# Kernel optimization log

Measured on AMD Instinct MI355X. Metric: run time of the kernel, lower is better.

The kernel has to match this reference:

```python
import jax, jax.numpy as jnp
import numpy as np

HID = 2048 * 3  # infl_ratio = 3
EPS = 1e-5
P_DROP = 0.5


def sign_ste(x):
    # straight-through binarization: sign in fwd, identity in bwd
    return x + jax.lax.stop_gradient(jnp.sign(x) - x)


def batchnorm(x, g, b):
    # training-mode BatchNorm1d: batch stats, biased variance
    m = jnp.mean(x, axis=0)
    v = jnp.mean((x - m) ** 2, axis=0)
    return g * (x - m) / jnp.sqrt(v + EPS) + b


def hardtanh(x):
    return jnp.clip(x, -1.0, 1.0)


def dropout(x, u):
    # u ~ U[0,1); keep where u >= p, scale by 1/(1-p)
    return jnp.where(u >= P_DROP, x / (1.0 - P_DROP), 0.0)


def setup_inputs() -> dict:
    key = jax.random.key(0)
    ks = jax.random.split(key, 16)
    B = 512
    d = {}
    d['x'] = jax.random.normal(ks[0], (B, 784), dtype=jnp.float32)
    d['drop_mask_bin'] = jax.random.uniform(ks[1], (B, HID), dtype=jnp.float32)
    d['drop_mask_real'] = jax.random.uniform(ks[2], (B, HID), dtype=jnp.float32)
    s1 = 1.0 / np.sqrt(784)
    sh = 1.0 / np.sqrt(HID)
    d['w1'] = jax.random.uniform(ks[3], (HID, 784), jnp.float32, -s1, s1)
    d['b1'] = jax.random.uniform(ks[4], (HID,), jnp.float32, -s1, s1)
    d['w2'] = jax.random.uniform(ks[5], (HID, HID), jnp.float32, -sh, sh)
    d['b2'] = jax.random.uniform(ks[6], (HID,), jnp.float32, -sh, sh)
    d['w3'] = jax.random.uniform(ks[7], (HID, HID), jnp.float32, -sh, sh)
    d['b3'] = jax.random.uniform(ks[8], (HID,), jnp.float32, -sh, sh)
    d['w4'] = jax.random.uniform(ks[9], (10, HID), jnp.float32, -sh, sh)
    d['b4'] = jax.random.uniform(ks[10], (10,), jnp.float32, -sh, sh)
    for i, k in zip((1, 2, 3), (ks[11], ks[12], ks[13])):
        d[f'g{i}'] = jnp.ones((HID,), jnp.float32)
        d[f'be{i}'] = jnp.zeros((HID,), jnp.float32)
    return d


def reference(x, drop_mask_bin, drop_mask_real, w1, b1, w2, b2, w3, b3, w4, b4,
              g1, be1, g2, be2, g3, be3):
    sg = jax.lax.stop_gradient
    # layer 1: input dim 784 -> input NOT binarized; weights binarized
    Bout1 = x @ sign_ste(w1).T + b1
    Rout1 = sg(x @ w1.T + b1)
    Bout1 = hardtanh(batchnorm(Bout1, g1, be1))
    Rout1 = sg(hardtanh(batchnorm(Rout1, g1, be1)))
    # layer 2: binarize activations and weights on binary path
    Bout2 = sign_ste(Bout1) @ sign_ste(w2).T + b2
    Rout2 = sg(Rout1 @ w2.T + b2)
    Bout2 = hardtanh(batchnorm(Bout2, g2, be2))
    Rout2 = sg(hardtanh(batchnorm(Rout2, g2, be2)))
    # layer 3 + dropout
    Bout3 = sign_ste(Bout2) @ sign_ste(w3).T + b3
    Rout3 = sg(Rout2 @ w3.T + b3)
    Bout3 = hardtanh(batchnorm(dropout(Bout3, drop_mask_bin), g3, be3))
    Rout3 = sg(hardtanh(batchnorm(dropout(Rout3, drop_mask_real), g3, be3)))
    # classifier (real-valued Linear)
    out = Bout3 @ w4.T + b4
    logp = jax.nn.log_softmax(out, axis=1)
    return (logp, out, Bout1, Rout1, Bout2, Rout2, Bout3, Rout3)
```

## Files before the change

### kernel.cpp

```cpp
#include <hip/hip_runtime.h>


typedef _Float16 f16x8 __attribute__((ext_vector_type(8)));
typedef _Float16 f16x4 __attribute__((ext_vector_type(4)));
typedef float f32x4 __attribute__((ext_vector_type(4)));
typedef int i32x4 __attribute__((ext_vector_type(4)));

#define MFMA16(a, b, c) __builtin_amdgcn_mfma_f32_16x16x32_f16((a), (b), (c), 0, 0, 0)
#define MFMAI8K32(a, b, c) __builtin_amdgcn_mfma_i32_16x16x32_i8((a), (b), (c), 0, 0, 0)
#define MFMAI8K64(a, b, c) __builtin_amdgcn_mfma_i32_16x16x64_i8((a), (b), (c), 0, 0, 0)

#define HIDC 6144
#define BATCH 512

#define OFF_XH    0ull
#define OFF_Z1LO  851968ull
#define OFF_SB8   13434880ull
#define OFF_RF    16580608ull
#define OFF_STATS 22872064ull
#define OFF_PPART 23068672ull
#define OFF_ZPB   24641536ull
#define OFF_ZPR   37224448ull
#define OFF_W1V   49807360ull
#define OFF_WV    60030976ull
#define OFF_WS8   135528448ull
#define WS_NEED   173277184ull

#define A8_STRIDE 425984ull

__device__ __forceinline__ void load_lds16(const void* g, char* lds) {
  __builtin_amdgcn_global_load_lds((const __attribute__((address_space(1))) void*)g,
                                   (__attribute__((address_space(3))) void*)lds, 16, 0, 0);
}

__global__ __launch_bounds__(256) void k_prep_x(const float* __restrict__ x,
                                                _Float16* __restrict__ xh) {
  int idx = blockIdx.x * 256 + threadIdx.x;
  if (idx >= 512 * 208) return;
  int row = idx / 208, c4 = idx - row * 208;
  f16x4 h;
  if (c4 < 196) {
    float4 v = *(const float4*)(x + (size_t)row * 784 + c4 * 4);
    h[0] = (_Float16)v.x; h[1] = (_Float16)v.y; h[2] = (_Float16)v.z; h[3] = (_Float16)v.w;
  } else {
    h[0] = (_Float16)0.f; h[1] = (_Float16)0.f; h[2] = (_Float16)0.f; h[3] = (_Float16)0.f;
  }
  *(f16x4*)(xh + (size_t)row * 832 + c4 * 4) = h;
}

__global__ __launch_bounds__(256) void k_quant_x(const float* __restrict__ x,
                                                 char* __restrict__ a8) {
  int idx = blockIdx.x * 256 + threadIdx.x;
  if (idx >= 512 * 832) return;
  int row = idx / 832, k = idx - row * 832;
  float v = (k < 784) ? x[(size_t)row * 784 + k] : 0.f;
  int q = (int)lrintf(v * 16777216.0f);
  int d0 = ((q + 128) & 255) - 128; q = (q - d0) >> 8;
  int d1 = ((q + 128) & 255) - 128; q = (q - d1) >> 8;
  int d2 = ((q + 128) & 255) - 128; q = (q - d2) >> 8;
  a8[idx] = (char)d0;
  a8[A8_STRIDE + idx] = (char)d1;
  a8[2 * A8_STRIDE + idx] = (char)d2;
  a8[3 * A8_STRIDE + idx] = (char)q;
}

__global__ __launch_bounds__(256) void k_sign_w1(const float* __restrict__ w,
                                                 char* __restrict__ s1) {
  int idx = blockIdx.x * 256 + threadIdx.x;
  if (idx >= 6144 * 832) return;
  int r = idx / 832, k = idx - r * 832;
  char s = 0;
  if (k < 784) {
    float v = w[(size_t)r * 784 + k];
    s = v > 0.f ? 1 : (v < 0.f ? -1 : 0);
  }
  s1[idx] = s;
}

__global__ __launch_bounds__(256) void k_conv_w1(const float* __restrict__ w,
                                                 _Float16* __restrict__ wv) {
  int idx = blockIdx.x * 256 + threadIdx.x;
  if (idx >= 6144 * 104) return;
  int r = idx / 104, c8 = idx - r * 104;
  f16x8 hv;
  if (c8 < 98) {
    const float* s = w + (size_t)r * 784 + c8 * 8;
    float4 v0 = *(const float4*)s;
    float4 v1 = *(const float4*)(s + 4);
    float a[8] = {v0.x, v0.y, v0.z, v0.w, v1.x, v1.y, v1.z, v1.w};
#pragma unroll
    for (int e = 0; e < 8; ++e) hv[e] = (_Float16)a[e];
  } else {
#pragma unroll
    for (int e = 0; e < 8; ++e) hv[e] = (_Float16)0.f;
  }
  *(f16x8*)(wv + (size_t)r * 832 + c8 * 8) = hv;
}

__global__ __launch_bounds__(256) void k_conv_w23(const float* __restrict__ w,
                                                  _Float16* __restrict__ wv,
                                                  char* __restrict__ ws8) {
  int idx = blockIdx.x * 256 + threadIdx.x;
  size_t o8 = (size_t)idx * 8;
  const float* s = w + o8;
  float4 v0 = *(const float4*)s;
  float4 v1 = *(const float4*)(s + 4);
  float a[8] = {v0.x, v0.y, v0.z, v0.w, v1.x, v1.y, v1.z, v1.w};
  f16x8 hv;
  unsigned long long sbits = 0;
#pragma unroll
  for (int e = 0; e < 8; ++e) {
    hv[e] = (_Float16)a[e];
    char sg = a[e] > 0.f ? 1 : (a[e] < 0.f ? -1 : 0);
    sbits |= ((unsigned long long)(unsigned char)sg) << (8 * e);
  }
  *(f16x8*)(wv + o8) = hv;
  *(unsigned long long*)(ws8 + o8) = sbits;
}

__global__ __launch_bounds__(256) void k_gemm_i8(const char* __restrict__ a8,
                                                 const char* __restrict__ s1,
                                                 int* __restrict__ D0,
                                                 int* __restrict__ D1,
                                                 int* __restrict__ D2,
                                                 int* __restrict__ D3) {
  __shared__ __align__(16) char smem[16384];
  const int z = blockIdx.z;
  const char* A = a8 + (size_t)z * A8_STRIDE;
  int* C = D0;
  if (z == 1) C = D1;
  if (z == 2) C = D2;
  if (z == 3) C = D3;
  const int t = threadIdx.x;
  const int lane = t & 63, wid = t >> 6;
  const int wm = wid >> 1, wn = wid & 1;
  const int bn = blockIdx.x, bm = blockIdx.y;

  i32x4 acc[4][4];
#pragma unroll
  for (int mf = 0; mf < 4; ++mf)
#pragma unroll
    for (int nf = 0; nf < 4; ++nf) acc[mf][nf] = (i32x4){0, 0, 0, 0};

  for (int kt = 0; kt < 13; ++kt) {
    const int k0 = kt * 64;
#pragma unroll
    for (int i = 0; i < 2; ++i) {
      int p = i * 256 + t;
      int r = p >> 2, c16 = p & 3;
      load_lds16(A + (size_t)(bm * 128 + r) * 832 + k0 + c16 * 16, smem + p * 16);
    }
#pragma unroll
    for (int i = 0; i < 2; ++i) {
      int p = i * 256 + t;
      int r = p >> 2, c16 = p & 3;
      load_lds16(s1 + (size_t)(bn * 128 + r) * 832 + k0 + c16 * 16, smem + 8192 + p * 16);
    }
    __syncthreads();
#pragma unroll
    for (int kk = 0; kk < 2; ++kk) {
      long av[4], bv[4];
#pragma unroll
      for (int mf = 0; mf < 4; ++mf) {
        int r = wm * 64 + mf * 16 + (lane & 15);
        av[mf] = *(const long*)(smem + r * 64 + kk * 32 + (lane >> 4) * 8);
      }
#pragma unroll
      for (int nf = 0; nf < 4; ++nf) {
        int r = wn * 64 + nf * 16 + (lane & 15);
        bv[nf] = *(const long*)(smem + 8192 + r * 64 + kk * 32 + (lane >> 4) * 8);
      }
#pragma unroll
      for (int mf = 0; mf < 4; ++mf)
#pragma unroll
        for (int nf = 0; nf < 4; ++nf) acc[mf][nf] = MFMAI8K32(av[mf], bv[nf], acc[mf][nf]);
    }
    __syncthreads();
  }
#pragma unroll
  for (int mf = 0; mf < 4; ++mf)
#pragma unroll
    for (int nf = 0; nf < 4; ++nf) {
      int col = bn * 128 + wn * 64 + nf * 16 + (lane & 15);
      int row0 = bm * 128 + wm * 64 + mf * 16 + ((lane >> 4) << 2);
#pragma unroll
      for (int rr = 0; rr < 4; ++rr) {
        C[(size_t)(row0 + rr) * HIDC + col] = acc[mf][nf][rr];
      }
    }
}

__global__ __launch_bounds__(256) void k_combine1(const int* __restrict__ D0,
                                                  const int* __restrict__ D1,
                                                  const int* __restrict__ D2,
                                                  const int* __restrict__ D3,
                                                  float* __restrict__ Zhi,
                                                  float* __restrict__ Zlo) {
  size_t i4 = ((size_t)blockIdx.x * 256 + threadIdx.x) * 4;
  i32x4 v0 = *(const i32x4*)(D0 + i4);
  i32x4 v1 = *(const i32x4*)(D1 + i4);
  i32x4 v2 = *(const i32x4*)(D2 + i4);
  i32x4 v3 = *(const i32x4*)(D3 + i4);
  float4 hi, lo;
  float* hp = &hi.x;
  float* lp = &lo.x;
#pragma unroll
  for (int e = 0; e < 4; ++e) {
    double zv = (((double)v3[e] * 256.0 + (double)v2[e]) * 256.0 + (double)v1[e]) * 256.0 +
                (double)v0[e];
    zv *= (1.0 / 16777216.0);
    float h = (float)zv;
    hp[e] = h;
    lp[e] = (float)(zv - (double)h);
  }
  *(float4*)(Zhi + i4) = hi;
  *(float4*)(Zlo + i4) = lo;
}

struct MixJob {
  const void* A;
  const void* B;
  float* C;
  int K;
  int kstart;
  int ksteps;
  int is8;
};
struct Mix4 { MixJob j[4]; };

__global__ __launch_bounds__(256) void k_gemm_mix(Mix4 P) {
  __shared__ __align__(16) char smem[32768];
  MixJob J = P.j[0];
  if (blockIdx.z == 1) J = P.j[1];
  if (blockIdx.z == 2) J = P.j[2];
  if (blockIdx.z == 3) J = P.j[3];
  const int t = threadIdx.x;
  const int lane = t & 63, wid = t >> 6;
  const int wm = wid >> 1, wn = wid & 1;
  const int bn = blockIdx.x, bm = blockIdx.y;
  const size_t K = (size_t)J.K;

  if (J.is8) {
    const char* A = (const char*)J.A;
    const char* B = (const char*)J.B;
    i32x4 acc[4][4];
#pragma unroll
    for (int mf = 0; mf < 4; ++mf)
#pragma unroll
      for (int nf = 0; nf < 4; ++nf) acc[mf][nf] = (i32x4){0, 0, 0, 0};

    for (int kt = 0; kt < J.ksteps; ++kt) {
      const int k0 = J.kstart + kt * 128;
#pragma unroll
      for (int i = 0; i < 4; ++i) {
        int p = i * 256 + t;
        int r = p >> 3, c16 = p & 7;
        load_lds16(A + (size_t)(bm * 128 + r) * K + k0 + c16 * 16, smem + p * 16);
      }
#pragma unroll
      for (int i = 0; i < 4; ++i) {
        int p = i * 256 + t;
        int r = p >> 3, c16 = p & 7;
        load_lds16(B + (size_t)(bn * 128 + r) * K + k0 + c16 * 16, smem + 16384 + p * 16);
      }
      __syncthreads();
#pragma unroll
      for (int kk = 0; kk < 2; ++kk) {
        i32x4 av[4], bv[4];
#pragma unroll
        for (int mf = 0; mf < 4; ++mf) {
          int r = wm * 64 + mf * 16 + (lane & 15);
          av[mf] = *(const i32x4*)(smem + r * 128 + kk * 64 + (lane >> 4) * 16);
        }
#pragma unroll
        for (int nf = 0; nf < 4; ++nf) {
          int r = wn * 64 + nf * 16 + (lane & 15);
          bv[nf] = *(const i32x4*)(smem + 16384 + r * 128 + kk * 64 + (lane >> 4) * 16);
        }
#pragma unroll
        for (int mf = 0; mf < 4; ++mf)
#pragma unroll
          for (int nf = 0; nf < 4; ++nf) acc[mf][nf] = MFMAI8K64(av[mf], bv[nf], acc[mf][nf]);
      }
      __syncthreads();
    }
#pragma unroll
    for (int mf = 0; mf < 4; ++mf)
#pragma unroll
      for (int nf = 0; nf < 4; ++nf) {
        int col = bn * 128 + wn * 64 + nf * 16 + (lane & 15);
        int row0 = bm * 128 + wm * 64 + mf * 16 + ((lane >> 4) << 2);
#pragma unroll
        for (int rr = 0; rr < 4; ++rr) {
          J.C[(size_t)(row0 + rr) * HIDC + col] = (float)acc[mf][nf][rr];
        }
      }
  } else {
    const _Float16* A = (const _Float16*)J.A;
    const _Float16* B = (const _Float16*)J.B;
    f32x4 acc[4][4];
#pragma unroll
    for (int mf = 0; mf < 4; ++mf)
#pragma unroll
      for (int nf = 0; nf < 4; ++nf) acc[mf][nf] = (f32x4){0.f, 0.f, 0.f, 0.f};

    for (int kt = 0; kt < J.ksteps; ++kt) {
      const int k0 = J.kstart + kt * 64;
#pragma unroll
      for (int i = 0; i < 4; ++i) {
        int p = i * 256 + t;
        int r = p >> 3, c16 = p & 7;
        load_lds16(A + (size_t)(bm * 128 + r) * K + k0 + c16 * 8, smem + p * 16);
      }
#pragma unroll
      for (int i = 0; i < 4; ++i) {
        int p = i * 256 + t;
        int r = p >> 3, c16 = p & 7;
        load_lds16(B + (size_t)(bn * 128 + r) * K + k0 + c16 * 8, smem + 16384 + p * 16);
      }
      __syncthreads();
#pragma unroll
      for (int kk = 0; kk < 2; ++kk) {
        f16x8 av[4], bv[4];
#pragma unroll
        for (int mf = 0; mf < 4; ++mf) {
          int r = wm * 64 + mf * 16 + (lane & 15);
          av[mf] = *(const f16x8*)(smem + r * 128 + kk * 64 + (lane >> 4) * 16);
        }
#pragma unroll
        for (int nf = 0; nf < 4; ++nf) {
          int r = wn * 64 + nf * 16 + (lane & 15);
          bv[nf] = *(const f16x8*)(smem + 16384 + r * 128 + kk * 64 + (lane >> 4) * 16);
        }
#pragma unroll
        for (int mf = 0; mf < 4; ++mf)
#pragma unroll
          for (int nf = 0; nf < 4; ++nf) acc[mf][nf] = MFMA16(av[mf], bv[nf], acc[mf][nf]);
      }
      __syncthreads();
    }
#pragma unroll
    for (int mf = 0; mf < 4; ++mf)
#pragma unroll
      for (int nf = 0; nf < 4; ++nf) {
        int col = bn * 128 + wn * 64 + nf * 16 + (lane & 15);
        int row0 = bm * 128 + wm * 64 + mf * 16 + ((lane >> 4) << 2);
#pragma unroll
        for (int rr = 0; rr < 4; ++rr) {
          J.C[(size_t)(row0 + rr) * HIDC + col] = acc[mf][nf][rr];
        }
      }
  }
}

struct StJob { const float* Z; const float* Zpart; const float* msk; };
struct St2 { StJob j[2]; const float* bias; int dodrop; double* ppart; };

__global__ __launch_bounds__(256) void k_stats_part(St2 P) {
  __shared__ double sm[4][64];
  __shared__ double sq[4][64];
  const int z = blockIdx.z;
  StJob J = z ? P.j[1] : P.j[0];
  const int li = threadIdx.x & 63, rg = threadIdx.x >> 6;
  const int col = blockIdx.x * 64 + li;
  const double bb = P.dodrop ? (double)P.bias[col] : 0.0;
  double s = 0.0, s2 = 0.0;
#pragma unroll 4
  for (int rr = 0; rr < 16; ++rr) {
    int r = blockIdx.y * 64 + rg * 16 + rr;
    size_t i = (size_t)r * HIDC + col;
    double v = (double)J.Z[i];
    if (J.Zpart) v += (double)J.Zpart[i];
    if (P.dodrop) v = (J.msk[i] >= 0.5f) ? 2.0 * (v + bb) : 0.0;
    s += v;
    s2 += v * v;
  }
  sm[rg][li] = s;
  sq[rg][li] = s2;
  __syncthreads();
  if (rg == 0) {
    double S = sm[0][li] + sm[1][li] + sm[2][li] + sm[3][li];
    double S2 = sq[0][li] + sq[1][li] + sq[2][li] + sq[3][li];
    size_t o = ((size_t)(z * 8 + blockIdx.y) * 2) * HIDC + col;
    P.ppart[o] = S;
    P.ppart[o + HIDC] = S2;
  }
}

__global__ __launch_bounds__(256) void k_stats_fin(const double* __restrict__ ppart,
                                                   double* __restrict__ stats) {
  const int z = blockIdx.z;
  const int c = blockIdx.x * 256 + threadIdx.x;
  double S = 0.0, S2 = 0.0;
#pragma unroll
  for (int y = 0; y < 8; ++y) {
    size_t o = ((size_t)(z * 8 + y) * 2) * HIDC + c;
    S += ppart[o];
    S2 += ppart[o + HIDC];
  }
  double m = S / 512.0;
  double var = S2 / 512.0 - m * m;
  stats[z * 2 * HIDC + c] = m;
  stats[z * 2 * HIDC + HIDC + c] = 1.0 / sqrt(var + 1e-5);
}

struct BnJob { float* Z; const float* Zpart; void* aux; const float* msk; int auxmode; };
struct Bn2 {
  BnJob j[2];
  const double* stats;
  const float* g; const float* be; const float* bias;
  int dodrop;
};

__global__ __launch_bounds__(256) void k_bn2(Bn2 P) {
  const int z = blockIdx.z;
  BnJob J = z ? P.j[1] : P.j[0];
  const double* m_arr = P.stats + (size_t)z * 2 * HIDC;
  const double* r_arr = m_arr + HIDC;
  int idx = blockIdx.x * 256 + threadIdx.x;
  int row = idx / 1536;
  int c4 = (idx - row * 1536) * 4;
  size_t base = (size_t)row * HIDC + c4;
  float4 zv = *(const float4*)(J.Z + base);
  float zz[4] = {zv.x, zv.y, zv.z, zv.w};
  float zl[4] = {0.f, 0.f, 0.f, 0.f};
  if (J.Zpart) {
    float4 t4 = *(const float4*)(J.Zpart + base);
    zl[0] = t4.x; zl[1] = t4.y; zl[2] = t4.z; zl[3] = t4.w;
  }
  float mk[4] = {1.f, 1.f, 1.f, 1.f};
  if (P.dodrop) {
    float4 t4 = *(const float4*)(J.msk + base);
    mk[0] = t4.x; mk[1] = t4.y; mk[2] = t4.z; mk[3] = t4.w;
  }
  float o[4];
  f16x4 a4;
  int sbits = 0;
#pragma unroll
  for (int e = 0; e < 4; ++e) {
    int c = c4 + e;
    double v = (double)zz[e] + (double)zl[e];
    if (P.dodrop) v = (mk[e] >= 0.5f) ? 2.0 * (v + (double)P.bias[c]) : 0.0;
    double bnv = (double)P.g[c] * ((v - m_arr[c]) * r_arr[c]) + (double)P.be[c];
    bnv = bnv > 1.0 ? 1.0 : (bnv < -1.0 ? -1.0 : bnv);
    o[e] = (float)bnv;
    char sg = bnv > 0.0 ? 1 : (bnv < 0.0 ? -1 : 0);
    sbits |= ((int)(unsigned char)sg) << (8 * e);
    a4[e] = (_Float16)o[e];
  }
  float4 ov = {o[0], o[1], o[2], o[3]};
  *(float4*)(J.Z + base) = ov;
  if (J.auxmode == 0) *(int*)((char*)J.aux + base) = sbits;
  if (J.auxmode == 1) *(f16x4*)((_Float16*)J.aux + base) = a4;
}

__global__ __launch_bounds__(256) void k_head(const float* __restrict__ B3,
                                              const float* __restrict__ w4,
                                              const float* __restrict__ b4,
                                              float* __restrict__ out,
                                              float* __restrict__ logp) {
  const int row = blockIdx.x, t = threadIdx.x;
  float acc[10];
#pragma unroll
  for (int j = 0; j < 10; ++j) acc[j] = 0.f;
  const float* a = B3 + (size_t)row * HIDC;
  for (int k4 = t; k4 < 1536; k4 += 256) {
    float4 av = *(const float4*)(a + k4 * 4);
#pragma unroll
    for (int j = 0; j < 10; ++j) {
      float4 wv = *(const float4*)(w4 + (size_t)j * HIDC + k4 * 4);
      acc[j] += av.x * wv.x + av.y * wv.y + av.z * wv.z + av.w * wv.w;
    }
  }
#pragma unroll
  for (int j = 0; j < 10; ++j)
    for (int off = 32; off; off >>= 1) acc[j] += __shfl_down(acc[j], off);
  __shared__ float sred[4][10];
  int wid = t >> 6, ln = t & 63;
  if (ln == 0)
#pragma unroll
    for (int j = 0; j < 10; ++j) sred[wid][j] = acc[j];
  __syncthreads();
  if (t == 0) {
    double o[10];
    double mx = -1e300;
#pragma unroll
    for (int j = 0; j < 10; ++j) {
      o[j] = (double)sred[0][j] + sred[1][j] + sred[2][j] + sred[3][j] + (double)b4[j];
      mx = o[j] > mx ? o[j] : mx;
    }
    double s = 0.0;
#pragma unroll
    for (int j = 0; j < 10; ++j) s += exp(o[j] - mx);
    double l = log(s) + mx;
#pragma unroll
    for (int j = 0; j < 10; ++j) {
      out[row * 10 + j] = (float)o[j];
      logp[row * 10 + j] = (float)(o[j] - l);
    }
  }
}

extern "C" void kernel_launch(void* const* d_in, const int* in_sizes, int n_in,
                              void* d_out, int out_size, void* d_ws, size_t ws_size,
                              hipStream_t stream) {
  const float* x   = (const float*)d_in[0];
  const float* mkb = (const float*)d_in[1];
  const float* mkr = (const float*)d_in[2];
  const float* w1  = (const float*)d_in[3];
  const float* w2  = (const float*)d_in[5];
  const float* w3  = (const float*)d_in[7];
  const float* b3  = (const float*)d_in[8];
  const float* w4  = (const float*)d_in[9];
  const float* b4  = (const float*)d_in[10];
  const float* g1  = (const float*)d_in[11]; const float* be1 = (const float*)d_in[12];
  const float* g2  = (const float*)d_in[13]; const float* be2 = (const float*)d_in[14];
  const float* g3  = (const float*)d_in[15]; const float* be3 = (const float*)d_in[16];

  float* outp = (float*)d_out;
  float* logp = outp;
  float* outo = outp + 5120;
  float* B1 = outp + 10240;
  float* R1 = outp + 3155968;
  float* B2 = outp + 6301696;
  float* R2 = outp + 9447424;
  float* B3 = outp + 12593152;
  float* R3 = outp + 15738880;

  char* ws = (char*)d_ws;
  _Float16* xh  = (_Float16*)(ws + OFF_XH);
  float* z1lo   = (float*)(ws + OFF_Z1LO);
  char* sB8     = (char*)(ws + OFF_SB8);
  _Float16* rF  = (_Float16*)(ws + OFF_RF);
  double* stats = (double*)(ws + OFF_STATS);
  double* ppart = (double*)(ws + OFF_PPART);
  float* zpb    = (float*)(ws + OFF_ZPB);
  float* zpr    = (float*)(ws + OFF_ZPR);
  _Float16* w1v = (_Float16*)(ws + OFF_W1V);
  _Float16* wv  = (_Float16*)(ws + OFF_WV);
  char* ws8     = (char*)(ws + OFF_WS8);
  char* a8 = (char*)(ws + OFF_WS8);
  char* s1 = (char*)(ws + OFF_WS8 + 2097152ull);
  int* D0 = (int*)(ws + OFF_ZPB);
  int* D1 = (int*)(ws + OFF_ZPR);
  int* D2 = (int*)(ws + OFF_WV);
  int* D3 = (int*)(ws + OFF_WV + 12582912ull);

  k_prep_x<<<416, 256, 0, stream>>>(x, xh);
  k_conv_w1<<<2496, 256, 0, stream>>>(w1, w1v);
  k_quant_x<<<1664, 256, 0, stream>>>(x, a8);
  k_sign_w1<<<19968, 256, 0, stream>>>(w1, s1);
  k_gemm_i8<<<dim3(48, 4, 4), 256, 0, stream>>>(a8, s1, D0, D1, D2, D3);
  k_combine1<<<3072, 256, 0, stream>>>(D0, D1, D2, D3, B1, z1lo);
  {
    Mix4 P{};
    P.j[0] = {xh, w1v, R1, 832, 0, 13, 0};
    P.j[1] = P.j[0]; P.j[2] = P.j[0]; P.j[3] = P.j[0];
    k_gemm_mix<<<dim3(48, 4, 1), 256, 0, stream>>>(P);
  }
  {
    St2 S{}; S.j[0] = {B1, z1lo, nullptr}; S.j[1] = {R1, nullptr, nullptr};
    S.bias = nullptr; S.dodrop = 0; S.ppart = ppart;
    k_stats_part<<<dim3(96, 8, 2), 256, 0, stream>>>(S);
    k_stats_fin<<<dim3(24, 1, 2), 256, 0, stream>>>(ppart, stats);
    Bn2 B{}; B.j[0] = {B1, z1lo, sB8, nullptr, 0}; B.j[1] = {R1, nullptr, rF, nullptr, 1};
    B.stats = stats; B.g = g1; B.be = be1; B.bias = nullptr; B.dodrop = 0;
    k_bn2<<<dim3(3072, 1, 2), 256, 0, stream>>>(B);
  }
  k_conv_w23<<<18432, 256, 0, stream>>>(w2, wv, ws8);
  {
    Mix4 P{};
    P.j[0] = {sB8, ws8, B2, HIDC, 0, 24, 1};
    P.j[1] = {sB8, ws8, zpb, HIDC, 3072, 24, 1};
    P.j[2] = {rF, wv, R2, HIDC, 0, 48, 0};
    P.j[3] = {rF, wv, zpr, HIDC, 3072, 48, 0};
    k_gemm_mix<<<dim3(48, 4, 4), 256, 0, stream>>>(P);
  }
  {
    St2 S{}; S.j[0] = {B2, zpb, nullptr}; S.j[1] = {R2, zpr, nullptr};
    S.bias = nullptr; S.dodrop = 0; S.ppart = ppart;
    k_stats_part<<<dim3(96, 8, 2), 256, 0, stream>>>(S);
    k_stats_fin<<<dim3(24, 1, 2), 256, 0, stream>>>(ppart, stats);
    Bn2 B{}; B.j[0] = {B2, zpb, sB8, nullptr, 0}; B.j[1] = {R2, zpr, rF, nullptr, 1};
    B.stats = stats; B.g = g2; B.be = be2; B.bias = nullptr; B.dodrop = 0;
    k_bn2<<<dim3(3072, 1, 2), 256, 0, stream>>>(B);
  }
  k_conv_w23<<<18432, 256, 0, stream>>>(w3, wv, ws8);
  {
    Mix4 P{};
    P.j[0] = {sB8, ws8, B3, HIDC, 0, 24, 1};
    P.j[1] = {sB8, ws8, zpb, HIDC, 3072, 24, 1};
    P.j[2] = {rF, wv, R3, HIDC, 0, 48, 0};
    P.j[3] = {rF, wv, zpr, HIDC, 3072, 48, 0};
    k_gemm_mix<<<dim3(48, 4, 4), 256, 0, stream>>>(P);
  }
  {
    St2 S{}; S.j[0] = {B3, zpb, mkb}; S.j[1] = {R3, zpr, mkr};
    S.bias = b3; S.dodrop = 1; S.ppart = ppart;
    k_stats_part<<<dim3(96, 8, 2), 256, 0, stream>>>(S);
    k_stats_fin<<<dim3(24, 1, 2), 256, 0, stream>>>(ppart, stats);
    Bn2 B{}; B.j[0] = {B3, zpb, nullptr, mkb, 2}; B.j[1] = {R3, zpr, nullptr, mkr, 2};
    B.stats = stats; B.g = g3; B.be = be3; B.bias = b3; B.dodrop = 1;
    k_bn2<<<dim3(3072, 1, 2), 256, 0, stream>>>(B);
  }
  k_head<<<512, 256, 0, stream>>>(B3, w4, b4, outo, logp);
}
```

Measured before the change: 564.1 us.

## Merge layer-1 GEMMs into mixed launch and split real-path K four ways

Layer-1 input prep is fused so one kernel quantizes x and converts it to fp16, and one kernel writes both the sign and the fp16 copy of w1. The separate int8 GEMM kernel is dropped; its four limb GEMMs now run as jobs of the generic mixed GEMM kernel, with K padded to 896, in the same launch as the fp16 real-path GEMM. For layers 2 and 3 the real-path GEMM is split into four K-chunks instead of two, which doubles the number of blocks in flight. The cost is two more fp32 partial buffers that the stats and batchnorm kernels must read and sum, plus a larger workspace.

```diff
diff --git a/kernel.cpp b/kernel.cpp
--- a/kernel.cpp
+++ b/kernel.cpp
@@ -7,7 +7,6 @@
 typedef int i32x4 __attribute__((ext_vector_type(4)));
 
 #define MFMA16(a, b, c) __builtin_amdgcn_mfma_f32_16x16x32_f16((a), (b), (c), 0, 0, 0)
-#define MFMAI8K32(a, b, c) __builtin_amdgcn_mfma_i32_16x16x32_i8((a), (b), (c), 0, 0, 0)
 #define MFMAI8K64(a, b, c) __builtin_amdgcn_mfma_i32_16x16x64_i8((a), (b), (c), 0, 0, 0)
 
 #define HIDC 6144
@@ -21,38 +20,26 @@
 #define OFF_PPART 23068672ull
 #define OFF_ZPB   24641536ull
 #define OFF_ZPR   37224448ull
-#define OFF_W1V   49807360ull
-#define OFF_WV    60030976ull
-#define OFF_WS8   135528448ull
-#define WS_NEED   173277184ull
-
-#define A8_STRIDE 425984ull
+#define OFF_ZPR2  49807360ull
+#define OFF_ZPR3  62390272ull
+#define OFF_W1V   74973184ull
+#define OFF_WV    85196800ull
+#define OFF_WS8   160694272ull
+#define WS_NEED   198443008ull
+
+#define A8_STRIDE 458752ull
 
 __device__ __forceinline__ void load_lds16(const void* g, char* lds) {
   __builtin_amdgcn_global_load_lds((const __attribute__((address_space(1))) void*)g,
                                    (__attribute__((address_space(3))) void*)lds, 16, 0, 0);
 }
 
-__global__ __launch_bounds__(256) void k_prep_x(const float* __restrict__ x,
-                                                _Float16* __restrict__ xh) {
+__global__ __launch_bounds__(256) void k_prep_xq(const float* __restrict__ x,
+                                                 char* __restrict__ a8,
+                                                 _Float16* __restrict__ xh) {
   int idx = blockIdx.x * 256 + threadIdx.x;
-  if (idx >= 512 * 208) return;
-  int row = idx / 208, c4 = idx - row * 208;
-  f16x4 h;
-  if (c4 < 196) {
-    float4 v = *(const float4*)(x + (size_t)row * 784 + c4 * 4);
-    h[0] = (_Float16)v.x; h[1] = (_Float16)v.y; h[2] = (_Float16)v.z; h[3] = (_Float16)v.w;
-  } else {
-    h[0] = (_Float16)0.f; h[1] = (_Float16)0.f; h[2] = (_Float16)0.f; h[3] = (_Float16)0.f;
-  }
-  *(f16x4*)(xh + (size_t)row * 832 + c4 * 4) = h;
-}
-
-__global__ __launch_bounds__(256) void k_quant_x(const float* __restrict__ x,
-                                                 char* __restrict__ a8) {
-  int idx = blockIdx.x * 256 + threadIdx.x;
-  if (idx >= 512 * 832) return;
-  int row = idx / 832, k = idx - row * 832;
+  if (idx >= 512 * 896) return;
+  int row = idx / 896, k = idx - row * 896;
   float v = (k < 784) ? x[(size_t)row * 784 + k] : 0.f;
   int q = (int)lrintf(v * 16777216.0f);
   int d0 = ((q + 128) & 255) - 128; q = (q - d0) >> 8;
@@ -62,39 +49,18 @@
   a8[A8_STRIDE + idx] = (char)d1;
   a8[2 * A8_STRIDE + idx] = (char)d2;
   a8[3 * A8_STRIDE + idx] = (char)q;
-}
-
-__global__ __launch_bounds__(256) void k_sign_w1(const float* __restrict__ w,
-                                                 char* __restrict__ s1) {
+  if (k < 832) xh[(size_t)row * 832 + k] = (_Float16)v;
+}
+
+__global__ __launch_bounds__(256) void k_prep_w1(const float* __restrict__ w,
+                                                 char* __restrict__ s1,
+                                                 _Float16* __restrict__ w1v) {
   int idx = blockIdx.x * 256 + threadIdx.x;
-  if (idx >= 6144 * 832) return;
-  int r = idx / 832, k = idx - r * 832;
-  char s = 0;
-  if (k < 784) {
-    float v = w[(size_t)r * 784 + k];
-    s = v > 0.f ? 1 : (v < 0.f ? -1 : 0);
-  }
-  s1[idx] = s;
-}
-
-__global__ __launch_bounds__(256) void k_conv_w1(const float* __restrict__ w,
-                                                 _Float16* __restrict__ wv) {
-  int idx = blockIdx.x * 256 + threadIdx.x;
-  if (idx >= 6144 * 104) return;
-  int r = idx / 104, c8 = idx - r * 104;
-  f16x8 hv;
-  if (c8 < 98) {
-    const float* s = w + (size_t)r * 784 + c8 * 8;
-    float4 v0 = *(const float4*)s;
-    float4 v1 = *(const float4*)(s + 4);
-    float a[8] = {v0.x, v0.y, v0.z, v0.w, v1.x, v1.y, v1.z, v1.w};
-#pragma unroll
-    for (int e = 0; e < 8; ++e) hv[e] = (_Float16)a[e];
-  } else {
-#pragma unroll
-    for (int e = 0; e < 8; ++e) hv[e] = (_Float16)0.f;
-  }
-  *(f16x8*)(wv + (size_t)r * 832 + c8 * 8) = hv;
+  if (idx >= 6144 * 896) return;
+  int r = idx / 896, k = idx - r * 896;
+  float v = (k < 784) ? w[(size_t)r * 784 + k] : 0.f;
+  s1[idx] = v > 0.f ? 1 : (v < 0.f ? -1 : 0);
+  if (k < 832) w1v[(size_t)r * 832 + k] = (_Float16)v;
 }
 
 __global__ __launch_bounds__(256) void k_conv_w23(const float* __restrict__ w,
@@ -118,105 +84,6 @@
   *(unsigned long long*)(ws8 + o8) = sbits;
 }
 
-__global__ __launch_bounds__(256) void k_gemm_i8(const char* __restrict__ a8,
-                                                 const char* __restrict__ s1,
-                                                 int* __restrict__ D0,
-                                                 int* __restrict__ D1,
-                                                 int* __restrict__ D2,
-                                                 int* __restrict__ D3) {
-  __shared__ __align__(16) char smem[16384];
-  const int z = blockIdx.z;
-  const char* A = a8 + (size_t)z * A8_STRIDE;
-  int* C = D0;
-  if (z == 1) C = D1;
-  if (z == 2) C = D2;
-  if (z == 3) C = D3;
-  const int t = threadIdx.x;
-  const int lane = t & 63, wid = t >> 6;
-  const int wm = wid >> 1, wn = wid & 1;
-  const int bn = blockIdx.x, bm = blockIdx.y;
-
-  i32x4 acc[4][4];
-#pragma unroll
-  for (int mf = 0; mf < 4; ++mf)
-#pragma unroll
-    for (int nf = 0; nf < 4; ++nf) acc[mf][nf] = (i32x4){0, 0, 0, 0};
-
-  for (int kt = 0; kt < 13; ++kt) {
-    const int k0 = kt * 64;
-#pragma unroll
-    for (int i = 0; i < 2; ++i) {
-      int p = i * 256 + t;
-      int r = p >> 2, c16 = p & 3;
-      load_lds16(A + (size_t)(bm * 128 + r) * 832 + k0 + c16 * 16, smem + p * 16);
-    }
-#pragma unroll
-    for (int i = 0; i < 2; ++i) {
-      int p = i * 256 + t;
-      int r = p >> 2, c16 = p & 3;
-      load_lds16(s1 + (size_t)(bn * 128 + r) * 832 + k0 + c16 * 16, smem + 8192 + p * 16);
-    }
-    __syncthreads();
-#pragma unroll
-    for (int kk = 0; kk < 2; ++kk) {
-      long av[4], bv[4];
-#pragma unroll
-      for (int mf = 0; mf < 4; ++mf) {
-        int r = wm * 64 + mf * 16 + (lane & 15);
-        av[mf] = *(const long*)(smem + r * 64 + kk * 32 + (lane >> 4) * 8);
-      }
-#pragma unroll
-      for (int nf = 0; nf < 4; ++nf) {
-        int r = wn * 64 + nf * 16 + (lane & 15);
-        bv[nf] = *(const long*)(smem + 8192 + r * 64 + kk * 32 + (lane >> 4) * 8);
-      }
-#pragma unroll
-      for (int mf = 0; mf < 4; ++mf)
-#pragma unroll
-        for (int nf = 0; nf < 4; ++nf) acc[mf][nf] = MFMAI8K32(av[mf], bv[nf], acc[mf][nf]);
-    }
-    __syncthreads();
-  }
-#pragma unroll
-  for (int mf = 0; mf < 4; ++mf)
-#pragma unroll
-    for (int nf = 0; nf < 4; ++nf) {
-      int col = bn * 128 + wn * 64 + nf * 16 + (lane & 15);
-      int row0 = bm * 128 + wm * 64 + mf * 16 + ((lane >> 4) << 2);
-#pragma unroll
-      for (int rr = 0; rr < 4; ++rr) {
-        C[(size_t)(row0 + rr) * HIDC + col] = acc[mf][nf][rr];
-      }
-    }
-}
-
-__global__ __launch_bounds__(256) void k_combine1(const int* __restrict__ D0,
-                                                  const int* __restrict__ D1,
-                                                  const int* __restrict__ D2,
-                                                  const int* __restrict__ D3,
-                                                  float* __restrict__ Zhi,
-                                                  float* __restrict__ Zlo) {
-  size_t i4 = ((size_t)blockIdx.x * 256 + threadIdx.x) * 4;
-  i32x4 v0 = *(const i32x4*)(D0 + i4);
-  i32x4 v1 = *(const i32x4*)(D1 + i4);
-  i32x4 v2 = *(const i32x4*)(D2 + i4);
-  i32x4 v3 = *(const i32x4*)(D3 + i4);
-  float4 hi, lo;
-  float* hp = &hi.x;
-  float* lp = &lo.x;
-#pragma unroll
-  for (int e = 0; e < 4; ++e) {
-    double zv = (((double)v3[e] * 256.0 + (double)v2[e]) * 256.0 + (double)v1[e]) * 256.0 +
-                (double)v0[e];
-    zv *= (1.0 / 16777216.0);
-    float h = (float)zv;
-    hp[e] = h;
-    lp[e] = (float)(zv - (double)h);
-  }
-  *(float4*)(Zhi + i4) = hi;
-  *(float4*)(Zlo + i4) = lo;
-}
-
 struct MixJob {
   const void* A;
   const void* B;
@@ -226,14 +93,16 @@
   int ksteps;
   int is8;
 };
-struct Mix4 { MixJob j[4]; };
-
-__global__ __launch_bounds__(256) void k_gemm_mix(Mix4 P) {
+struct Mix6 { MixJob j[6]; };
+
+__global__ __launch_bounds__(256) void k_gemm_mix(Mix6 P) {
   __shared__ __align__(16) char smem[32768];
   MixJob J = P.j[0];
   if (blockIdx.z == 1) J = P.j[1];
   if (blockIdx.z == 2) J = P.j[2];
   if (blockIdx.z == 3) J = P.j[3];
+  if (blockIdx.z == 4) J = P.j[4];
+  if (blockIdx.z == 5) J = P.j[5];
   const int t = threadIdx.x;
   const int lane = t & 63, wid = t >> 6;
   const int wm = wid >> 1, wn = wid & 1;
@@ -353,7 +222,39 @@
   }
 }
 
-struct StJob { const float* Z; const float* Zpart; const float* msk; };
+__global__ __launch_bounds__(256) void k_combine1(const float* __restrict__ D0,
+                                                  const float* __restrict__ D1,
+                                                  const float* __restrict__ D2,
+                                                  const float* __restrict__ D3,
+                                                  float* __restrict__ Zhi,
+                                                  float* __restrict__ Zlo) {
+  size_t i4 = ((size_t)blockIdx.x * 256 + threadIdx.x) * 4;
+  float4 v0 = *(const float4*)(D0 + i4);
+  float4 v1 = *(const float4*)(D1 + i4);
+  float4 v2 = *(const float4*)(D2 + i4);
+  float4 v3 = *(const float4*)(D3 + i4);
+  const float* p0 = &v0.x;
+  const float* p1 = &v1.x;
+  const float* p2 = &v2.x;
+  const float* p3 = &v3.x;
+  float4 hi, lo;
+  float* hp = &hi.x;
+  float* lp = &lo.x;
+#pragma unroll
+  for (int e = 0; e < 4; ++e) {
+    double zv = (((double)p3[e] * 256.0 + (double)p2[e]) * 256.0 + (double)p1[e]) * 256.0 +
+                (double)p0[e];
+    zv *= (1.0 / 16777216.0);
+    float h = (float)zv;
+    hp[e] = h;
+    lp[e] = (float)(zv - (double)h);
+  }
+  *(float4*)(Zhi + i4) = hi;
+  *(float4*)(Zlo + i4) = lo;
+}
+
+struct StJob { const float* Z; const float* Zp0; const float* Zp1; const float* Zp2;
+               const float* msk; };
 struct St2 { StJob j[2]; const float* bias; int dodrop; double* ppart; };
 
 __global__ __launch_bounds__(256) void k_stats_part(St2 P) {
@@ -370,7 +271,9 @@
     int r = blockIdx.y * 64 + rg * 16 + rr;
     size_t i = (size_t)r * HIDC + col;
     double v = (double)J.Z[i];
-    if (J.Zpart) v += (double)J.Zpart[i];
+    if (J.Zp0) v += (double)J.Zp0[i];
+    if (J.Zp1) v += (double)J.Zp1[i];
+    if (J.Zp2) v += (double)J.Zp2[i];
     if (P.dodrop) v = (J.msk[i] >= 0.5f) ? 2.0 * (v + bb) : 0.0;
     s += v;
     s2 += v * v;
@@ -404,7 +307,8 @@
   stats[z * 2 * HIDC + HIDC + c] = 1.0 / sqrt(var + 1e-5);
 }
 
-struct BnJob { float* Z; const float* Zpart; void* aux; const float* msk; int auxmode; };
+struct BnJob { float* Z; const float* Zp0; const float* Zp1; const float* Zp2;
+               void* aux; const float* msk; int auxmode; };
 struct Bn2 {
   BnJob j[2];
   const double* stats;
@@ -423,10 +327,18 @@
   size_t base = (size_t)row * HIDC + c4;
   float4 zv = *(const float4*)(J.Z + base);
   float zz[4] = {zv.x, zv.y, zv.z, zv.w};
-  float zl[4] = {0.f, 0.f, 0.f, 0.f};
-  if (J.Zpart) {
-    float4 t4 = *(const float4*)(J.Zpart + base);
-    zl[0] = t4.x; zl[1] = t4.y; zl[2] = t4.z; zl[3] = t4.w;
+  double ex[4] = {0.0, 0.0, 0.0, 0.0};
+  if (J.Zp0) {
+    float4 t4 = *(const float4*)(J.Zp0 + base);
+    ex[0] += t4.x; ex[1] += t4.y; ex[2] += t4.z; ex[3] += t4.w;
+  }
+  if (J.Zp1) {
+    float4 t4 = *(const float4*)(J.Zp1 + base);
+    ex[0] += t4.x; ex[1] += t4.y; ex[2] += t4.z; ex[3] += t4.w;
+  }
+  if (J.Zp2) {
+    float4 t4 = *(const float4*)(J.Zp2 + base);
+    ex[0] += t4.x; ex[1] += t4.y; ex[2] += t4.z; ex[3] += t4.w;
   }
   float mk[4] = {1.f, 1.f, 1.f, 1.f};
   if (P.dodrop) {
@@ -439,7 +351,7 @@
 #pragma unroll
   for (int e = 0; e < 4; ++e) {
     int c = c4 + e;
-    double v = (double)zz[e] + (double)zl[e];
+    double v = (double)zz[e] + ex[e];
     if (P.dodrop) v = (mk[e] >= 0.5f) ? 2.0 * (v + (double)P.bias[c]) : 0.0;
     double bnv = (double)P.g[c] * ((v - m_arr[c]) * r_arr[c]) + (double)P.be[c];
     bnv = bnv > 1.0 ? 1.0 : (bnv < -1.0 ? -1.0 : bnv);
@@ -536,70 +448,85 @@
   double* ppart = (double*)(ws + OFF_PPART);
   float* zpb    = (float*)(ws + OFF_ZPB);
   float* zpr    = (float*)(ws + OFF_ZPR);
+  float* zpr2   = (float*)(ws + OFF_ZPR2);
+  float* zpr3   = (float*)(ws + OFF_ZPR3);
   _Float16* w1v = (_Float16*)(ws + OFF_W1V);
   _Float16* wv  = (_Float16*)(ws + OFF_WV);
   char* ws8     = (char*)(ws + OFF_WS8);
   char* a8 = (char*)(ws + OFF_WS8);
-  char* s1 = (char*)(ws + OFF_WS8 + 2097152ull);
-  int* D0 = (int*)(ws + OFF_ZPB);
-  int* D1 = (int*)(ws + OFF_ZPR);
-  int* D2 = (int*)(ws + OFF_WV);
-  int* D3 = (int*)(ws + OFF_WV + 12582912ull);
-
-  k_prep_x<<<416, 256, 0, stream>>>(x, xh);
-  k_conv_w1<<<2496, 256, 0, stream>>>(w1, w1v);
-  k_quant_x<<<1664, 256, 0, stream>>>(x, a8);
-  k_sign_w1<<<19968, 256, 0, stream>>>(w1, s1);
-  k_gemm_i8<<<dim3(48, 4, 4), 256, 0, stream>>>(a8, s1, D0, D1, D2, D3);
-  k_combine1<<<3072, 256, 0, stream>>>(D0, D1, D2, D3, B1, z1lo);
+  char* s1 = (char*)(ws + OFF_WS8 + 4ull * A8_STRIDE);
+
+  k_prep_xq<<<1792, 256, 0, stream>>>(x, a8, xh);
+  k_prep_w1<<<21504, 256, 0, stream>>>(w1, s1, w1v);
   {
-    Mix4 P{};
-    P.j[0] = {xh, w1v, R1, 832, 0, 13, 0};
-    P.j[1] = P.j[0]; P.j[2] = P.j[0]; P.j[3] = P.j[0];
-    k_gemm_mix<<<dim3(48, 4, 1), 256, 0, stream>>>(P);
-  }
+    Mix6 P{};
+    P.j[0] = {a8,                 s1, zpb,  896, 0, 7, 1};
+    P.j[1] = {a8 + A8_STRIDE,     s1, zpr,  896, 0, 7, 1};
+    P.j[2] = {a8 + 2 * A8_STRIDE, s1, zpr2, 896, 0, 7, 1};
+    P.j[3] = {a8 + 3 * A8_STRIDE, s1, zpr3, 896, 0, 7, 1};
+    P.j[4] = {xh, w1v, R1, 832, 0, 13, 0};
+    P.j[5] = P.j[4];
+    k_gemm_mix<<<dim3(48, 4, 5), 256, 0, stream>>>(P);
+  }
+  k_combine1<<<3072, 256, 0, stream>>>(zpb, zpr, zpr2, zpr3, B1, z1lo);
   {
-    St2 S{}; S.j[0] = {B1, z1lo, nullptr}; S.j[1] = {R1, nullptr, nullptr};
+    St2 S{};
+    S.j[0] = {B1, z1lo, nullptr, nullptr, nullptr};
+    S.j[1] = {R1, nullptr, nullptr, nullptr, nullptr};
     S.bias = nullptr; S.dodrop = 0; S.ppart = ppart;
     k_stats_part<<<dim3(96, 8, 2), 256, 0, stream>>>(S);
     k_stats_fin<<<dim3(24, 1, 2), 256, 0, stream>>>(ppart, stats);
-    Bn2 B{}; B.j[0] = {B1, z1lo, sB8, nullptr, 0}; B.j[1] = {R1, nullptr, rF, nullptr, 1};
+    Bn2 B{};
+    B.j[0] = {B1, z1lo, nullptr, nullptr, sB8, nullptr, 0};
+    B.j[1] = {R1, nullptr, nullptr, nullptr, rF, nullptr, 1};
     B.stats = stats; B.g = g1; B.be = be1; B.bias = nullptr; B.dodrop = 0;
     k_bn2<<<dim3(3072, 1, 2), 256, 0, stream>>>(B);
   }
   k_conv_w23<<<18432, 256, 0, stream>>>(w2, wv, ws8);
   {
-    Mix4 P{};
-    P.j[0] = {sB8, ws8, B2, HIDC, 0, 24, 1};
-    P.j[1] = {sB8, ws8, zpb, HIDC, 3072, 24, 1};
-    P.j[2] = {rF, wv, R2, HIDC, 0, 48, 0};
-    P.j[3] = {rF, wv, zpr, HIDC, 3072, 48, 0};
-    k_gemm_mix<<<dim3(48, 4, 4), 256, 0, stream>>>(P);
+    Mix6 P{};
+    P.j[0] = {sB8, ws8, B2,   HIDC, 0,    24, 1};
+    P.j[1] = {sB8, ws8, zpb,  HIDC, 3072, 24, 1};
+    P.j[2] = {rF,  wv,  R2,   HIDC, 0,    24, 0};
+    P.j[3] = {rF,  wv,  zpr,  HIDC, 1536, 24, 0};
+    P.j[4] = {rF,  wv,  zpr2, HIDC, 3072, 24, 0};
+    P.j[5] = {rF,  wv,  zpr3, HIDC, 4608, 24, 0};
+    k_gemm_mix<<<dim3(48, 4, 6), 256, 0, stream>>>(P);
   }
   {
-    St2 S{}; S.j[0] = {B2, zpb, nullptr}; S.j[1] = {R2, zpr, nullptr};
+    St2 S{};
+    S.j[0] = {B2, zpb, nullptr, nullptr, nullptr};
+    S.j[1] = {R2, zpr, zpr2, zpr3, nullptr};
     S.bias = nullptr; S.dodrop = 0; S.ppart = ppart;
     k_stats_part<<<dim3(96, 8, 2), 256, 0, stream>>>(S);
     k_stats_fin<<<dim3(24, 1, 2), 256, 0, stream>>>(ppart, stats);
-    Bn2 B{}; B.j[0] = {B2, zpb, sB8, nullptr, 0}; B.j[1] = {R2, zpr, rF, nullptr, 1};
+    Bn2 B{};
+    B.j[0] = {B2, zpb, nullptr, nullptr, sB8, nullptr, 0};
+    B.j[1] = {R2, zpr, zpr2, zpr3, rF, nullptr, 1};
     B.stats = stats; B.g = g2; B.be = be2; B.bias = nullptr; B.dodrop = 0;
     k_bn2<<<dim3(3072, 1, 2), 256, 0, stream>>>(B);
   }
   k_conv_w23<<<18432, 256, 0, stream>>>(w3, wv, ws8);
   {
-    Mix4 P{};
-    P.j[0] = {sB8, ws8, B3, HIDC, 0, 24, 1};
-    P.j[1] = {sB8, ws8, zpb, HIDC, 3072, 24, 1};
-    P.j[2] = {rF, wv, R3, HIDC, 0, 48, 0};
-    P.j[3] = {rF, wv, zpr, HIDC, 3072, 48, 0};
-    k_gemm_mix<<<dim3(48, 4, 4), 256, 0, stream>>>(P);
+    Mix6 P{};
+    P.j[0] = {sB8, ws8, B3,   HIDC, 0,    24, 1};
+    P.j[1] = {sB8, ws8, zpb,  HIDC, 3072, 24, 1};
+    P.j[2] = {rF,  wv,  R3,   HIDC, 0,    24, 0};
+    P.j[3] = {rF,  wv,  zpr,  HIDC, 1536, 24, 0};
+    P.j[4] = {rF,  wv,  zpr2, HIDC, 3072, 24, 0};
+    P.j[5] = {rF,  wv,  zpr3, HIDC, 4608, 24, 0};
+    k_gemm_mix<<<dim3(48, 4, 6), 256, 0, stream>>>(P);
   }
   {
-    St2 S{}; S.j[0] = {B3, zpb, mkb}; S.j[1] = {R3, zpr, mkr};
+    St2 S{};
+    S.j[0] = {B3, zpb, nullptr, nullptr, mkb};
+    S.j[1] = {R3, zpr, zpr2, zpr3, mkr};
     S.bias = b3; S.dodrop = 1; S.ppart = ppart;
     k_stats_part<<<dim3(96, 8, 2), 256, 0, stream>>>(S);
     k_stats_fin<<<dim3(24, 1, 2), 256, 0, stream>>>(ppart, stats);
-    Bn2 B{}; B.j[0] = {B3, zpb, nullptr, mkb, 2}; B.j[1] = {R3, zpr, nullptr, mkr, 2};
+    Bn2 B{};
+    B.j[0] = {B3, zpb, nullptr, nullptr, nullptr, mkb, 2};
+    B.j[1] = {R3, zpr, zpr2, zpr3, nullptr, mkr, 2};
     B.stats = stats; B.g = g3; B.be = be3; B.bias = b3; B.dodrop = 1;
     k_bn2<<<dim3(3072, 1, 2), 256, 0, stream>>>(B);
   }
```

Measured after the change: 559.7 us. Within noise of the previous version (-0.8%).
